# Kernel tuning notes

Hardware: AMD Instinct MI355X
Metric: run time of the kernel (lower is better)

Reference implementation:

```python
import jax, jax.numpy as jnp
from jax import lax
import numpy as np

T, B, DIN, NQ = 256, 2048, 128, 16  # hidden_dim == n_qubits (required by module math)


def setup_inputs() -> dict:
    key = jax.random.key(0)
    k1, k2, k3 = jax.random.split(key, 3)
    inputs = jax.random.normal(k1, (T, B, DIN), dtype=jnp.float32)
    # stacked params for the 4 gates: forget, input, update, output
    W = jax.random.normal(k2, (4, NQ, DIN + NQ), dtype=jnp.float32) * 0.1
    b = jnp.zeros((4, NQ), dtype=jnp.float32)
    theta = jax.random.normal(k3, (4, NQ), dtype=jnp.float32)
    return {"inputs": inputs, "W": W, "b": b, "theta": theta}


def reference(inputs, W, b, theta):
    # Analytic simulation of each QGate circuit:
    #   RX(x_i) then RX(theta_i) on wire i  ->  product state, <Z_i> = cos(x_i + theta_i)
    #   CNOT chain (0->1, 1->2, ...): Heisenberg picture maps Z_k -> Z_0 Z_1 ... Z_k,
    Tn, Bn, _ = inputs.shape
    nq = theta.shape[-1]
    h0 = jnp.zeros((Bn, nq), dtype=inputs.dtype)
    c0 = jnp.zeros((Bn, nq), dtype=inputs.dtype)

    def step(carry, x):
        hx, cx = carry
        combined = jnp.concatenate([x, hx], axis=1)              # [B, Din+H]
        z = jnp.einsum('bd,gnd->bgn', combined, W) + b           # [B, 4, nq]
        q = jnp.cumprod(jnp.cos(z + theta), axis=-1)             # quantum gate expectations
        f = jax.nn.sigmoid(q[:, 0])
        i = jax.nn.sigmoid(q[:, 1])
        g = jnp.tanh(q[:, 2])
        o = jax.nn.sigmoid(q[:, 3])
        cx = f * cx + i * g
        hx = o * jnp.tanh(cx)
        return (hx, cx), hx

    (hx, cx), outputs = lax.scan(step, (h0, c0), inputs)
    return outputs, hx, cx
```

## Files before the change

kernel.cpp:

```cpp
#include <hip/hip_runtime.h>
#include <hip/hip_bf16.h>
#include <stdint.h>


#define T_STEPS 256
#define BATCH   2048
#define DIN     128
#define NQ      16
#define DTOT    144
#define NTILE   32
#define ZROW    66

typedef __attribute__((ext_vector_type(8))) short bf16x8;
typedef __attribute__((ext_vector_type(4))) float f32x4;
typedef __attribute__((ext_vector_type(2))) int   int2v;

#if defined(__has_builtin)
#if __has_builtin(__builtin_amdgcn_permlane16_swap) && __has_builtin(__builtin_amdgcn_permlane32_swap)
#define USE_PLSWAP 1
#endif
#endif
#ifndef USE_PLSWAP
#define USE_PLSWAP 0
#endif

__device__ __forceinline__ float bf2f(unsigned short u) {
    union { unsigned int i; float f; } v; v.i = ((unsigned int)u) << 16; return v.f;
}
__device__ __forceinline__ unsigned short f2bf(float f) {
    union { float f; unsigned int i; } v; v.f = f;
    unsigned int i = v.i;
    unsigned int r = i + 0x7fffu + ((i >> 16) & 1u);
    return (unsigned short)(r >> 16);
}
__device__ __forceinline__ float ldval(const float* p) { return *p; }
__device__ __forceinline__ float ldval(const unsigned short* p) { return bf2f(*p); }

__device__ __forceinline__ int detect_bf16(const unsigned int* __restrict__ xw, int lane) {
    int cnt = 0;
#pragma unroll
    for (int i = 0; i < 4; ++i) {
        unsigned int w = xw[lane + i * 64];
        unsigned int e = (w >> 7) & 0xFFu;
        cnt += (e >= 100u && e <= 140u) ? 1 : 0;
    }
#pragma unroll
    for (int d = 32; d > 0; d >>= 1) cnt += __shfl_down(cnt, d, 64);
    int tot = __shfl(cnt, 0, 64);
    return (tot >= 140) ? 1 : 0;
}

template <int CTRL>
__device__ __forceinline__ float dpp_sh(float v) {
    int r = __builtin_amdgcn_update_dpp(__builtin_bit_cast(int, 1.0f),
                                        __builtin_bit_cast(int, v),
                                        CTRL, 0xF, 0xF, false);
    return __builtin_bit_cast(float, r);
}

__device__ __forceinline__ float dot1(float h, float cur, const float (&Wp)[16]) {
    float a0 = cur, a1, a2, a3;
    asm volatile(
        "s_nop 1\n\t"
        "v_fmac_f32 %0, %4, %5\n\t"
        "v_mul_f32_dpp %1, %4, %6 row_ror:4 row_mask:0xf bank_mask:0xf\n\t"
        "v_mul_f32_dpp %2, %4, %7 row_ror:8 row_mask:0xf bank_mask:0xf\n\t"
        "v_mul_f32_dpp %3, %4, %8 row_ror:12 row_mask:0xf bank_mask:0xf\n\t"
        "v_fmac_f32_dpp %0, %4, %9 row_ror:1 row_mask:0xf bank_mask:0xf\n\t"
        "v_fmac_f32_dpp %1, %4, %10 row_ror:5 row_mask:0xf bank_mask:0xf\n\t"
        "v_fmac_f32_dpp %2, %4, %11 row_ror:9 row_mask:0xf bank_mask:0xf\n\t"
        "v_fmac_f32_dpp %3, %4, %12 row_ror:13 row_mask:0xf bank_mask:0xf\n\t"
        "v_fmac_f32_dpp %0, %4, %13 row_ror:2 row_mask:0xf bank_mask:0xf\n\t"
        "v_fmac_f32_dpp %1, %4, %14 row_ror:6 row_mask:0xf bank_mask:0xf\n\t"
        "v_fmac_f32_dpp %2, %4, %15 row_ror:10 row_mask:0xf bank_mask:0xf\n\t"
        "v_fmac_f32_dpp %3, %4, %16 row_ror:14 row_mask:0xf bank_mask:0xf\n\t"
        "v_fmac_f32_dpp %0, %4, %17 row_ror:3 row_mask:0xf bank_mask:0xf\n\t"
        "v_fmac_f32_dpp %1, %4, %18 row_ror:7 row_mask:0xf bank_mask:0xf\n\t"
        "v_fmac_f32_dpp %2, %4, %19 row_ror:11 row_mask:0xf bank_mask:0xf\n\t"
        "v_fmac_f32_dpp %3, %4, %20 row_ror:15 row_mask:0xf bank_mask:0xf"
        : "+v"(a0), "=&v"(a1), "=&v"(a2), "=&v"(a3)
        : "v"(h), "v"(Wp[0]), "v"(Wp[4]), "v"(Wp[8]), "v"(Wp[12]),
          "v"(Wp[1]), "v"(Wp[5]), "v"(Wp[9]), "v"(Wp[13]),
          "v"(Wp[2]), "v"(Wp[6]), "v"(Wp[10]), "v"(Wp[14]),
          "v"(Wp[3]), "v"(Wp[7]), "v"(Wp[11]), "v"(Wp[15]));
    return (a0 + a1) + (a2 + a3);
}

template <int BASE>
__device__ __forceinline__ float cosprefix(float z) {
    float cz = __cosf(z);
    cz *= dpp_sh<BASE + 1>(cz);
    cz *= dpp_sh<BASE + 2>(cz);
    cz *= dpp_sh<BASE + 4>(cz);
    cz *= dpp_sh<BASE + 8>(cz);
    return cz;
}

__device__ __forceinline__ void gex(float s, bool m0, bool m1,
                                    int a_f, int a_i, int a_g, int a_o,
                                    float& fv, float& iv, float& gv, float& ov)
{
#if USE_PLSWAP
    int si = __builtin_bit_cast(int, s);
    int2v e1 = __builtin_amdgcn_permlane16_swap(si, si, false, false);
    int c1i = m0 ? e1[0] : e1[1];
    int2v e2 = __builtin_amdgcn_permlane32_swap(si, si, false, false);
    int c2i = m1 ? e2[0] : e2[1];
    int2v e3 = __builtin_amdgcn_permlane16_swap(c2i, c2i, false, false);
    int c3i = m0 ? e3[0] : e3[1];
    float C0 = s;
    float C1 = __builtin_bit_cast(float, c1i);
    float C2 = __builtin_bit_cast(float, c2i);
    float C3 = __builtin_bit_cast(float, c3i);
    float P  = m1 ? C2 : C0;
    float Q  = m1 ? C3 : C1;
    float R_ = m1 ? C0 : C2;
    float S_ = m1 ? C1 : C3;
    fv = m0 ? Q  : P;
    iv = m0 ? P  : Q;
    gv = m0 ? S_ : R_;
    ov = m0 ? R_ : S_;
#else
    int si = __builtin_bit_cast(int, s);
    fv = __builtin_bit_cast(float, __builtin_amdgcn_ds_bpermute(a_f, si));
    iv = __builtin_bit_cast(float, __builtin_amdgcn_ds_bpermute(a_i, si));
    gv = __builtin_bit_cast(float, __builtin_amdgcn_ds_bpermute(a_g, si));
    ov = __builtin_bit_cast(float, __builtin_amdgcn_ds_bpermute(a_o, si));
#endif
}

__device__ __forceinline__ void tail1(int t, int g, int n, float cz,
                                      float& h, float& c, float& hs, int b,
                                      bool m0, bool m1,
                                      float kexp, float ksc, float koff,
                                      int a_f, int a_i, int a_g, int a_o,
                                      float* __restrict__ out)
{
    float e = __builtin_amdgcn_exp2f(cz * kexp);
    float rr = __builtin_amdgcn_rcpf(1.f + e);
    float s = fmaf(ksc, rr, koff);

    float fv, iv, gv, ov;
    gex(s, m0, m1, a_f, a_i, a_g, a_o, fv, iv, gv, ov);

    c = fmaf(fv, c, iv * gv);
    float e2 = __builtin_amdgcn_exp2f(c * -2.885390082f);
    float tc = fmaf(2.f, __builtin_amdgcn_rcpf(1.f + e2), -1.f);
    h = ov * tc;

    if ((t & 3) == g) hs = h;
    if ((t & 3) == 3)
        out[(size_t)(t - 3 + g) * (BATCH * NQ) + (size_t)b * NQ + n] = hs;
}

template <int BASE, typename InT>
__device__ __forceinline__ void fused_main(
    const InT* __restrict__ x, const InT* __restrict__ W,
    const InT* __restrict__ bv, const InT* __restrict__ th,
    float* __restrict__ out, int bA, int w, int lane,
    const float (&Wp)[16], float (*zt)[ZROW],
    bf16x8 (*wfh)[64], bf16x8 (*wfl)[64])
{
    const int m = lane & 15, quad = lane >> 4;
    const int g = quad, n = m;
    const int bB = bA + 1;
    const bool m0 = (g & 1) != 0, m1 = (g & 2) != 0;
    const float kexp = (g == 2) ? -2.885390082f : -1.442695041f;
    const float ksc  = (g == 2) ? 2.f : 1.f;
    const float koff = (g == 2) ? -1.f : 0.f;
    const int a_f = n << 2, a_i = (16 + n) << 2, a_g = (32 + n) << 2, a_o = (48 + n) << 2;

    if constexpr (sizeof(InT) == 2) {
#pragma unroll
        for (int nb = 0; nb < 4; ++nb)
            wfh[w * 4 + nb][lane] = *(const bf16x8*)((const unsigned short*)W +
                                    (size_t)(nb * 16 + m) * DTOT + w * 32 + quad * 8);
    } else {
#pragma unroll
        for (int nb = 0; nb < 4; ++nb) {
            const float* p = (const float*)W + (size_t)(nb * 16 + m) * DTOT + w * 32 + quad * 8;
            bf16x8 ah, al;
#pragma unroll
            for (int j = 0; j < 8; ++j) {
                float wv = p[j];
                unsigned short hh = f2bf(wv);
                ah[j] = (short)hh;
                al[j] = (short)f2bf(wv - bf2f(hh));
            }
            wfh[w * 4 + nb][lane] = ah;
            wfl[w * 4 + nb][lane] = al;
        }
    }
    const float bias = ldval(bv + lane) + ldval(th + lane);
    __syncthreads();

    const InT* xbase = x + ((size_t)(m & 7) * BATCH + (size_t)(bA + (m >> 3))) * DIN + quad * 8;

    f32x4 rx[8]; bf16x8 rbx[4];
    auto LOAD = [&](int tl) {
        const InT* p = xbase + (size_t)tl * ((size_t)8 * BATCH * DIN);
#pragma unroll
        for (int kt = 0; kt < 4; ++kt) {
            if constexpr (sizeof(InT) == 2) {
                rbx[kt] = *(const bf16x8*)(p + kt * 32);
            } else {
                rx[2 * kt]     = *(const f32x4*)((const float*)p + kt * 32);
                rx[2 * kt + 1] = *(const f32x4*)((const float*)p + kt * 32 + 4);
            }
        }
    };
    auto PRODUCE = [&]() {
        f32x4 acc[4] = {};
#pragma unroll
        for (int kt = 0; kt < 4; ++kt) {
            if constexpr (sizeof(InT) == 2) {
#pragma unroll
                for (int nb = 0; nb < 4; ++nb)
                    acc[nb] = __builtin_amdgcn_mfma_f32_16x16x32_bf16(rbx[kt], wfh[kt * 4 + nb][lane], acc[nb], 0, 0, 0);
            } else {
                bf16x8 ah, al;
#pragma unroll
                for (int j = 0; j < 8; ++j) {
                    float xv = rx[2 * kt + (j >> 2)][j & 3];
                    unsigned short hh = f2bf(xv);
                    ah[j] = (short)hh;
                    al[j] = (short)f2bf(xv - bf2f(hh));
                }
#pragma unroll
                for (int nb = 0; nb < 4; ++nb)
                    acc[nb] = __builtin_amdgcn_mfma_f32_16x16x32_bf16(ah, wfh[kt * 4 + nb][lane], acc[nb], 0, 0, 0);
#pragma unroll
                for (int nb = 0; nb < 4; ++nb)
                    acc[nb] = __builtin_amdgcn_mfma_f32_16x16x32_bf16(al, wfh[kt * 4 + nb][lane], acc[nb], 0, 0, 0);
#pragma unroll
                for (int nb = 0; nb < 4; ++nb)
                    acc[nb] = __builtin_amdgcn_mfma_f32_16x16x32_bf16(ah, wfl[kt * 4 + nb][lane], acc[nb], 0, 0, 0);
            }
        }
#pragma unroll
        for (int nb = 0; nb < 4; ++nb)
#pragma unroll
            for (int r = 0; r < 4; ++r)
                zt[quad * 4 + r][nb * 16 + m] = acc[nb][r];
    };

    float hA = 0.f, cA = 0.f, hsA = 0.f;
    float hB = 0.f, cB = 0.f, hsB = 0.f;
    float zrA[8], zrB[8];

    LOAD(0);
    PRODUCE();
    LOAD(1);
#pragma unroll
    for (int j = 0; j < 8; ++j) zrA[j] = zt[j][lane] + bias;
#pragma unroll
    for (int j = 0; j < 8; ++j) zrB[j] = zt[8 + j][lane] + bias;

    float zA = dot1(hA, zrA[0], Wp);
    float czB = 0.f;

#pragma unroll 1
    for (int tl = 0; tl < NTILE; ++tl) {
        if (tl < NTILE - 1) PRODUCE();
        if (tl < NTILE - 2) LOAD(tl + 2);
#pragma unroll
        for (int j = 0; j < 8; ++j) {
            const int t = tl * 8 + j;
            float czA = cosprefix<BASE>(zA);
            if (j != 0 || tl != 0)
                tail1(t - 1, g, n, czB, hB, cB, hsB, bB, m0, m1,
                      kexp, ksc, koff, a_f, a_i, a_g, a_o, out);
            float zB = dot1(hB, zrB[j], Wp);
            czB = cosprefix<BASE>(zB);
            tail1(t, g, n, czA, hA, cA, hsA, bA, m0, m1,
                  kexp, ksc, koff, a_f, a_i, a_g, a_o, out);
            if (j < 7) zA = dot1(hA, zrA[j + 1], Wp);
        }
        if (tl < NTILE - 1) {
#pragma unroll
            for (int j = 0; j < 8; ++j) zrA[j] = zt[j][lane] + bias;
#pragma unroll
            for (int j = 0; j < 8; ++j) zrB[j] = zt[8 + j][lane] + bias;
            zA = dot1(hA, zrA[0], Wp);
        }
    }
    tail1(T_STEPS - 1, g, n, czB, hB, cB, hsB, bB, m0, m1,
          kexp, ksc, koff, a_f, a_i, a_g, a_o, out);

    if (g == 0) {
        out[(size_t)T_STEPS * BATCH * NQ + (size_t)bA * NQ + n] = hA;
        out[(size_t)T_STEPS * BATCH * NQ + (size_t)BATCH * NQ + (size_t)bA * NQ + n] = cA;
        out[(size_t)T_STEPS * BATCH * NQ + (size_t)bB * NQ + n] = hB;
        out[(size_t)T_STEPS * BATCH * NQ + (size_t)BATCH * NQ + (size_t)bB * NQ + n] = cB;
    }
}

__global__ __launch_bounds__(256, 1) void qlstm_fused(
    const void* __restrict__ x_, const void* __restrict__ W_,
    const void* __restrict__ b_, const void* __restrict__ th_,
    float* __restrict__ out)
{
    __shared__ float  zw[4][16][ZROW];
    __shared__ bf16x8 wfh[16][64];
    __shared__ bf16x8 wfl[16][64];

    const int lane = threadIdx.x & 63;
    const int w    = threadIdx.x >> 6;
    const int bA   = (blockIdx.x * 4 + w) * 2;
    const int n    = lane & 15;

    const int isbf = __builtin_amdgcn_readfirstlane(detect_bf16((const unsigned int*)x_, lane));

    int pr  = __builtin_amdgcn_update_dpp(0, lane, 0x121, 0xF, 0xF, false);
    int p0r = __shfl(pr, 0, 64);
    const int d = (p0r == 1) ? 1 : 15;

    float Wp[16];
    if (isbf) {
        const unsigned short* W = (const unsigned short*)W_;
#pragma unroll
        for (int k = 0; k < 16; ++k)
            Wp[k] = bf2f(W[(size_t)lane * DTOT + DIN + ((n + k * d) & 15)]);
    } else {
        const float* W = (const float*)W_;
#pragma unroll
        for (int k = 0; k < 16; ++k)
            Wp[k] = W[(size_t)lane * DTOT + DIN + ((n + k * d) & 15)];
    }

    int probe = __builtin_amdgcn_update_dpp(999, lane, 0x111, 0xF, 0xF, false);
    int p2 = __shfl(probe, 2, 64);

    if (isbf) {
        if (p2 == 1) fused_main<0x110, unsigned short>((const unsigned short*)x_, (const unsigned short*)W_,
                                                       (const unsigned short*)b_, (const unsigned short*)th_,
                                                       out, bA, w, lane, Wp, zw[w], wfh, wfl);
        else         fused_main<0x100, unsigned short>((const unsigned short*)x_, (const unsigned short*)W_,
                                                       (const unsigned short*)b_, (const unsigned short*)th_,
                                                       out, bA, w, lane, Wp, zw[w], wfh, wfl);
    } else {
        if (p2 == 1) fused_main<0x110, float>((const float*)x_, (const float*)W_,
                                              (const float*)b_, (const float*)th_,
                                              out, bA, w, lane, Wp, zw[w], wfh, wfl);
        else         fused_main<0x100, float>((const float*)x_, (const float*)W_,
                                              (const float*)b_, (const float*)th_,
                                              out, bA, w, lane, Wp, zw[w], wfh, wfl);
    }
}

extern "C" void kernel_launch(void* const* d_in, const int* in_sizes, int n_in,
                              void* d_out, int out_size, void* d_ws, size_t ws_size,
                              hipStream_t stream) {
    const void* x  = d_in[0];
    const void* W  = d_in[1];
    const void* bv = d_in[2];
    const void* th = d_in[3];
    (void)d_ws; (void)ws_size;
    qlstm_fused<<<BATCH / 8, 256, 0, stream>>>(x, W, bv, th, (float*)d_out);
}
```

Baseline: 390.9 us.

## Overlap gate-exchange bpermutes with the other chain's dot product; use packed bf16 split

Replaces the permlane-swap gate exchange with ds_bpermute instructions issued inside the same inline-asm block as the DPP dot product of the interleaved second batch chain, so LDS permute latency is hidden behind the FMAs. The recurrent step is reorganised so that each chain's gate values are exchanged while the other chain computes its recurrent dot. The bf16 hi/lo split of fp32 inputs and weights now uses the packed v_cvt_pk_bf16_f32 instruction instead of manual rounding. The volatile asm with an explicit lgkmcnt wait constrains scheduling and adds LDS traffic on the critical path.

```diff
diff --git a/kernel.cpp b/kernel.cpp
--- a/kernel.cpp
+++ b/kernel.cpp
@@ -13,28 +13,28 @@
 
 typedef __attribute__((ext_vector_type(8))) short bf16x8;
 typedef __attribute__((ext_vector_type(4))) float f32x4;
-typedef __attribute__((ext_vector_type(2))) int   int2v;
-
-#if defined(__has_builtin)
-#if __has_builtin(__builtin_amdgcn_permlane16_swap) && __has_builtin(__builtin_amdgcn_permlane32_swap)
-#define USE_PLSWAP 1
-#endif
-#endif
-#ifndef USE_PLSWAP
-#define USE_PLSWAP 0
-#endif
+typedef __attribute__((ext_vector_type(4))) unsigned int u32x4;
 
 __device__ __forceinline__ float bf2f(unsigned short u) {
     union { unsigned int i; float f; } v; v.i = ((unsigned int)u) << 16; return v.f;
 }
-__device__ __forceinline__ unsigned short f2bf(float f) {
-    union { float f; unsigned int i; } v; v.f = f;
-    unsigned int i = v.i;
-    unsigned int r = i + 0x7fffu + ((i >> 16) & 1u);
-    return (unsigned short)(r >> 16);
-}
 __device__ __forceinline__ float ldval(const float* p) { return *p; }
 __device__ __forceinline__ float ldval(const unsigned short* p) { return bf2f(*p); }
+
+__device__ __forceinline__ unsigned int cvt_pk_bf16(float a, float b) {
+    unsigned int r;
+    asm("v_cvt_pk_bf16_f32 %0, %1, %2" : "=v"(r) : "v"(a), "v"(b));
+    return r;
+}
+struct bfpair { unsigned int hw, lw; };
+__device__ __forceinline__ bfpair split2(float x0, float x1) {
+    bfpair r;
+    r.hw = cvt_pk_bf16(x0, x1);
+    float r0 = __builtin_bit_cast(float, r.hw << 16);
+    float r1 = __builtin_bit_cast(float, r.hw & 0xffff0000u);
+    r.lw = cvt_pk_bf16(x0 - r0, x1 - r1);
+    return r;
+}
 
 __device__ __forceinline__ int detect_bf16(const unsigned int* __restrict__ xw, int lane) {
     int cnt = 0;
@@ -58,7 +58,22 @@
     return __builtin_bit_cast(float, r);
 }
 
-__device__ __forceinline__ float dot1(float h, float cur, const float (&Wp)[16]) {
+template <int BASE>
+__device__ __forceinline__ float cosprefix(float z) {
+    float cz = __cosf(z);
+    cz *= dpp_sh<BASE + 1>(cz);
+    cz *= dpp_sh<BASE + 2>(cz);
+    cz *= dpp_sh<BASE + 4>(cz);
+    cz *= dpp_sh<BASE + 8>(cz);
+    return cz;
+}
+__device__ __forceinline__ float nonlin(float cz, float kexp, float ksc, float koff) {
+    float e = __builtin_amdgcn_exp2f(cz * kexp);
+    float rr = __builtin_amdgcn_rcpf(1.f + e);
+    return fmaf(ksc, rr, koff);
+}
+
+__device__ __forceinline__ float dot_plain(float h, float cur, const float (&Wp)[16]) {
     float a0 = cur, a1, a2, a3;
     asm volatile(
         "s_nop 1\n\t"
@@ -86,71 +101,52 @@
     return (a0 + a1) + (a2 + a3);
 }
 
-template <int BASE>
-__device__ __forceinline__ float cosprefix(float z) {
-    float cz = __cosf(z);
-    cz *= dpp_sh<BASE + 1>(cz);
-    cz *= dpp_sh<BASE + 2>(cz);
-    cz *= dpp_sh<BASE + 4>(cz);
-    cz *= dpp_sh<BASE + 8>(cz);
-    return cz;
-}
-
-__device__ __forceinline__ void gex(float s, bool m0, bool m1,
+__device__ __forceinline__ float dot_gex(float h, float cur, const float (&Wp)[16],
+                                         float s_o, int a_f, int a_i, int a_g, int a_o,
+                                         float& fv, float& iv, float& gv, float& ov)
+{
+    float a0 = cur, a1, a2, a3;
+    asm volatile(
+        "ds_bpermute_b32 %1, %10, %9\n\t"
+        "ds_bpermute_b32 %2, %11, %9\n\t"
+        "ds_bpermute_b32 %3, %12, %9\n\t"
+        "ds_bpermute_b32 %4, %13, %9\n\t"
+        "v_fmac_f32 %0, %8, %14\n\t"
+        "v_mul_f32_dpp %5, %8, %15 row_ror:4 row_mask:0xf bank_mask:0xf\n\t"
+        "v_mul_f32_dpp %6, %8, %16 row_ror:8 row_mask:0xf bank_mask:0xf\n\t"
+        "v_mul_f32_dpp %7, %8, %17 row_ror:12 row_mask:0xf bank_mask:0xf\n\t"
+        "v_fmac_f32_dpp %0, %8, %18 row_ror:1 row_mask:0xf bank_mask:0xf\n\t"
+        "v_fmac_f32_dpp %5, %8, %19 row_ror:5 row_mask:0xf bank_mask:0xf\n\t"
+        "v_fmac_f32_dpp %6, %8, %20 row_ror:9 row_mask:0xf bank_mask:0xf\n\t"
+        "v_fmac_f32_dpp %7, %8, %21 row_ror:13 row_mask:0xf bank_mask:0xf\n\t"
+        "v_fmac_f32_dpp %0, %8, %22 row_ror:2 row_mask:0xf bank_mask:0xf\n\t"
+        "v_fmac_f32_dpp %5, %8, %23 row_ror:6 row_mask:0xf bank_mask:0xf\n\t"
+        "v_fmac_f32_dpp %6, %8, %24 row_ror:10 row_mask:0xf bank_mask:0xf\n\t"
+        "v_fmac_f32_dpp %7, %8, %25 row_ror:14 row_mask:0xf bank_mask:0xf\n\t"
+        "v_fmac_f32_dpp %0, %8, %26 row_ror:3 row_mask:0xf bank_mask:0xf\n\t"
+        "v_fmac_f32_dpp %5, %8, %27 row_ror:7 row_mask:0xf bank_mask:0xf\n\t"
+        "v_fmac_f32_dpp %6, %8, %28 row_ror:11 row_mask:0xf bank_mask:0xf\n\t"
+        "v_fmac_f32_dpp %7, %8, %29 row_ror:15 row_mask:0xf bank_mask:0xf\n\t"
+        "s_waitcnt lgkmcnt(0)"
+        : "+v"(a0), "=&v"(fv), "=&v"(iv), "=&v"(gv), "=&v"(ov),
+          "=&v"(a1), "=&v"(a2), "=&v"(a3)
+        : "v"(h), "v"(s_o), "v"(a_f), "v"(a_i), "v"(a_g), "v"(a_o),
+          "v"(Wp[0]), "v"(Wp[4]), "v"(Wp[8]), "v"(Wp[12]),
+          "v"(Wp[1]), "v"(Wp[5]), "v"(Wp[9]), "v"(Wp[13]),
+          "v"(Wp[2]), "v"(Wp[6]), "v"(Wp[10]), "v"(Wp[14]),
+          "v"(Wp[3]), "v"(Wp[7]), "v"(Wp[11]), "v"(Wp[15]));
+    return (a0 + a1) + (a2 + a3);
+}
+
+__device__ __forceinline__ void gex(float s,
                                     int a_f, int a_i, int a_g, int a_o,
                                     float& fv, float& iv, float& gv, float& ov)
 {
-#if USE_PLSWAP
-    int si = __builtin_bit_cast(int, s);
-    int2v e1 = __builtin_amdgcn_permlane16_swap(si, si, false, false);
-    int c1i = m0 ? e1[0] : e1[1];
-    int2v e2 = __builtin_amdgcn_permlane32_swap(si, si, false, false);
-    int c2i = m1 ? e2[0] : e2[1];
-    int2v e3 = __builtin_amdgcn_permlane16_swap(c2i, c2i, false, false);
-    int c3i = m0 ? e3[0] : e3[1];
-    float C0 = s;
-    float C1 = __builtin_bit_cast(float, c1i);
-    float C2 = __builtin_bit_cast(float, c2i);
-    float C3 = __builtin_bit_cast(float, c3i);
-    float P  = m1 ? C2 : C0;
-    float Q  = m1 ? C3 : C1;
-    float R_ = m1 ? C0 : C2;
-    float S_ = m1 ? C1 : C3;
-    fv = m0 ? Q  : P;
-    iv = m0 ? P  : Q;
-    gv = m0 ? S_ : R_;
-    ov = m0 ? R_ : S_;
-#else
     int si = __builtin_bit_cast(int, s);
     fv = __builtin_bit_cast(float, __builtin_amdgcn_ds_bpermute(a_f, si));
     iv = __builtin_bit_cast(float, __builtin_amdgcn_ds_bpermute(a_i, si));
     gv = __builtin_bit_cast(float, __builtin_amdgcn_ds_bpermute(a_g, si));
     ov = __builtin_bit_cast(float, __builtin_amdgcn_ds_bpermute(a_o, si));
-#endif
-}
-
-__device__ __forceinline__ void tail1(int t, int g, int n, float cz,
-                                      float& h, float& c, float& hs, int b,
-                                      bool m0, bool m1,
-                                      float kexp, float ksc, float koff,
-                                      int a_f, int a_i, int a_g, int a_o,
-                                      float* __restrict__ out)
-{
-    float e = __builtin_amdgcn_exp2f(cz * kexp);
-    float rr = __builtin_amdgcn_rcpf(1.f + e);
-    float s = fmaf(ksc, rr, koff);
-
-    float fv, iv, gv, ov;
-    gex(s, m0, m1, a_f, a_i, a_g, a_o, fv, iv, gv, ov);
-
-    c = fmaf(fv, c, iv * gv);
-    float e2 = __builtin_amdgcn_exp2f(c * -2.885390082f);
-    float tc = fmaf(2.f, __builtin_amdgcn_rcpf(1.f + e2), -1.f);
-    h = ov * tc;
-
-    if ((t & 3) == g) hs = h;
-    if ((t & 3) == 3)
-        out[(size_t)(t - 3 + g) * (BATCH * NQ) + (size_t)b * NQ + n] = hs;
 }
 
 template <int BASE, typename InT>
@@ -164,7 +160,6 @@
     const int m = lane & 15, quad = lane >> 4;
     const int g = quad, n = m;
     const int bB = bA + 1;
-    const bool m0 = (g & 1) != 0, m1 = (g & 2) != 0;
     const float kexp = (g == 2) ? -2.885390082f : -1.442695041f;
     const float ksc  = (g == 2) ? 2.f : 1.f;
     const float koff = (g == 2) ? -1.f : 0.f;
@@ -179,16 +174,15 @@
 #pragma unroll
         for (int nb = 0; nb < 4; ++nb) {
             const float* p = (const float*)W + (size_t)(nb * 16 + m) * DTOT + w * 32 + quad * 8;
-            bf16x8 ah, al;
-#pragma unroll
-            for (int j = 0; j < 8; ++j) {
-                float wv = p[j];
-                unsigned short hh = f2bf(wv);
-                ah[j] = (short)hh;
-                al[j] = (short)f2bf(wv - bf2f(hh));
-            }
-            wfh[w * 4 + nb][lane] = ah;
-            wfl[w * 4 + nb][lane] = al;
+            u32x4 hw_, lw_;
+#pragma unroll
+            for (int q = 0; q < 4; ++q) {
+                bfpair pr = split2(p[2 * q], p[2 * q + 1]);
+                hw_[q] = pr.hw;
+                lw_[q] = pr.lw;
+            }
+            wfh[w * 4 + nb][lane] = __builtin_bit_cast(bf16x8, hw_);
+            wfl[w * 4 + nb][lane] = __builtin_bit_cast(bf16x8, lw_);
         }
     }
     const float bias = ldval(bv + lane) + ldval(th + lane);
@@ -218,14 +212,17 @@
                 for (int nb = 0; nb < 4; ++nb)
                     acc[nb] = __builtin_amdgcn_mfma_f32_16x16x32_bf16(rbx[kt], wfh[kt * 4 + nb][lane], acc[nb], 0, 0, 0);
             } else {
-                bf16x8 ah, al;
-#pragma unroll
-                for (int j = 0; j < 8; ++j) {
-                    float xv = rx[2 * kt + (j >> 2)][j & 3];
-                    unsigned short hh = f2bf(xv);
-                    ah[j] = (short)hh;
-                    al[j] = (short)f2bf(xv - bf2f(hh));
+                u32x4 hw_, lw_;
+#pragma unroll
+                for (int q = 0; q < 4; ++q) {
+                    float x0 = rx[2 * kt + (q >> 1)][(q & 1) * 2];
+                    float x1 = rx[2 * kt + (q >> 1)][(q & 1) * 2 + 1];
+                    bfpair pr = split2(x0, x1);
+                    hw_[q] = pr.hw;
+                    lw_[q] = pr.lw;
                 }
+                bf16x8 ah = __builtin_bit_cast(bf16x8, hw_);
+                bf16x8 al = __builtin_bit_cast(bf16x8, lw_);
 #pragma unroll
                 for (int nb = 0; nb < 4; ++nb)
                     acc[nb] = __builtin_amdgcn_mfma_f32_16x16x32_bf16(ah, wfh[kt * 4 + nb][lane], acc[nb], 0, 0, 0);
@@ -246,6 +243,7 @@
 
     float hA = 0.f, cA = 0.f, hsA = 0.f;
     float hB = 0.f, cB = 0.f, hsB = 0.f;
+    float fvA, ivA, gvA, ovA, fvB = 0.f, ivB = 0.f, gvB = 0.f, ovB = 0.f;
     float zrA[8], zrB[8];
 
     LOAD(0);
@@ -256,8 +254,7 @@
 #pragma unroll
     for (int j = 0; j < 8; ++j) zrB[j] = zt[8 + j][lane] + bias;
 
-    float zA = dot1(hA, zrA[0], Wp);
-    float czB = 0.f;
+    float zA = dot_plain(hA, zrA[0], Wp);
 
 #pragma unroll 1
     for (int tl = 0; tl < NTILE; ++tl) {
@@ -267,25 +264,50 @@
         for (int j = 0; j < 8; ++j) {
             const int t = tl * 8 + j;
             float czA = cosprefix<BASE>(zA);
-            if (j != 0 || tl != 0)
-                tail1(t - 1, g, n, czB, hB, cB, hsB, bB, m0, m1,
-                      kexp, ksc, koff, a_f, a_i, a_g, a_o, out);
-            float zB = dot1(hB, zrB[j], Wp);
-            czB = cosprefix<BASE>(zB);
-            tail1(t, g, n, czA, hA, cA, hsA, bA, m0, m1,
-                  kexp, ksc, koff, a_f, a_i, a_g, a_o, out);
-            if (j < 7) zA = dot1(hA, zrA[j + 1], Wp);
+            float sA = nonlin(czA, kexp, ksc, koff);
+            if (j != 0 || tl != 0) {
+                cB = fmaf(fvB, cB, ivB * gvB);
+                float e2 = __builtin_amdgcn_exp2f(cB * -2.885390082f);
+                float tc = fmaf(2.f, __builtin_amdgcn_rcpf(1.f + e2), -1.f);
+                hB = ovB * tc;
+                if (((t - 1) & 3) == g) hsB = hB;
+                if (((t - 1) & 3) == 3)
+                    out[(size_t)(t - 4 + g) * (BATCH * NQ) + (size_t)bB * NQ + n] = hsB;
+            }
+            float zB = dot_gex(hB, zrB[j], Wp, sA, a_f, a_i, a_g, a_o,
+                               fvA, ivA, gvA, ovA);
+            float czB = cosprefix<BASE>(zB);
+            float sB = nonlin(czB, kexp, ksc, koff);
+            cA = fmaf(fvA, cA, ivA * gvA);
+            {
+                float e2 = __builtin_amdgcn_exp2f(cA * -2.885390082f);
+                float tc = fmaf(2.f, __builtin_amdgcn_rcpf(1.f + e2), -1.f);
+                hA = ovA * tc;
+            }
+            if ((t & 3) == g) hsA = hA;
+            if ((t & 3) == 3)
+                out[(size_t)(t - 3 + g) * (BATCH * NQ) + (size_t)bA * NQ + n] = hsA;
+            if (j < 7) {
+                zA = dot_gex(hA, zrA[j + 1], Wp, sB, a_f, a_i, a_g, a_o,
+                             fvB, ivB, gvB, ovB);
+            } else if (tl < NTILE - 1) {
+#pragma unroll
+                for (int k = 0; k < 8; ++k) zrA[k] = zt[k][lane] + bias;
+#pragma unroll
+                for (int k = 0; k < 8; ++k) zrB[k] = zt[8 + k][lane] + bias;
+                zA = dot_gex(hA, zrA[0], Wp, sB, a_f, a_i, a_g, a_o,
+                             fvB, ivB, gvB, ovB);
+            } else {
+                gex(sB, a_f, a_i, a_g, a_o, fvB, ivB, gvB, ovB);
+                cB = fmaf(fvB, cB, ivB * gvB);
+                float e2 = __builtin_amdgcn_exp2f(cB * -2.885390082f);
+                float tc = fmaf(2.f, __builtin_amdgcn_rcpf(1.f + e2), -1.f);
+                hB = ovB * tc;
+                if ((3) == g) hsB = hB;
+                out[(size_t)(252 + g) * (BATCH * NQ) + (size_t)bB * NQ + n] = hsB;
+            }
         }
-        if (tl < NTILE - 1) {
-#pragma unroll
-            for (int j = 0; j < 8; ++j) zrA[j] = zt[j][lane] + bias;
-#pragma unroll
-            for (int j = 0; j < 8; ++j) zrB[j] = zt[8 + j][lane] + bias;
-            zA = dot1(hA, zrA[0], Wp);
-        }
-    }
-    tail1(T_STEPS - 1, g, n, czB, hB, cB, hsB, bB, m0, m1,
-          kexp, ksc, koff, a_f, a_i, a_g, a_o, out);
+    }
 
     if (g == 0) {
         out[(size_t)T_STEPS * BATCH * NQ + (size_t)bA * NQ + n] = hA;
```

Result: faster. 380.6 us (-2.7%).
